# Performance work log

Hardware: AMD Instinct MI355X
Metric: run time of the kernel (lower is better)

Reference implementation:

```python
import jax, jax.numpy as jnp
import numpy as np

DIM = 128
HEADS = 4
CH = DIM // HEADS  # out_channels per head = 32
EDGE_DIM = 1
N_NODES = 50000
N_EDGES = 800000
NEG_SLOPE = 0.2
LN_EPS = 1e-5
SM_EPS = 1e-16  # PyG softmax denom eps


def setup_inputs() -> dict:
    key = jax.random.key(0)
    ks = jax.random.split(key, 10)
    x = jax.random.normal(ks[0], (N_NODES, DIM), dtype=jnp.float32)
    edge_index = jax.random.randint(ks[1], (2, N_EDGES), 0, N_NODES, dtype=jnp.int64)
    edge_attr = jax.random.normal(ks[2], (N_EDGES, EDGE_DIM), dtype=jnp.float32)
    s = 0.05
    W_l = jax.random.normal(ks[3], (DIM, HEADS * CH), dtype=jnp.float32) * s   # shared lin_l/lin_r (share_weights=True)
    b_l = jax.random.normal(ks[4], (HEADS * CH,), dtype=jnp.float32) * s
    W_e = jax.random.normal(ks[5], (EDGE_DIM, HEADS * CH), dtype=jnp.float32) * s  # lin_edge (no bias)
    att = jax.random.normal(ks[6], (HEADS, CH), dtype=jnp.float32) * s
    bias = jax.random.normal(ks[7], (HEADS * CH,), dtype=jnp.float32) * s      # conv output bias
    ln_gamma = jnp.ones((DIM,), dtype=jnp.float32)
    ln_beta = jnp.zeros((DIM,), dtype=jnp.float32)
    return {"x": x, "edge_index": edge_index, "edge_attr": edge_attr,
            "W_l": W_l, "b_l": b_l, "W_e": W_e, "att": att, "bias": bias,
            "ln_gamma": ln_gamma, "ln_beta": ln_beta}


def reference(x, edge_index, edge_attr, W_l, b_l, W_e, att, bias, ln_gamma, ln_beta):
    N = x.shape[0]
    src, dst = edge_index[0], edge_index[1]

    # --- GATv2Conv (share_weights=True, add_self_loops=False, edge_dim injection) ---
    xl = (x @ W_l + b_l).reshape(N, HEADS, CH)            # [N,H,C] (x_l == x_r)
    e = (edge_attr @ W_e).reshape(-1, HEADS, CH)          # [E,H,C]
    m = jax.nn.leaky_relu(xl[src] + xl[dst] + e, NEG_SLOPE)  # [E,H,C]
    alpha = jnp.einsum('ehc,hc->eh', m, att)              # [E,H]

    # segment softmax over destination node neighborhoods
    amax = jax.ops.segment_max(alpha, dst, num_segments=N)   # [N,H]
    ea = jnp.exp(alpha - amax[dst])                           # [E,H]
    denom = jax.ops.segment_sum(ea, dst, num_segments=N)      # [N,H]
    alpha = ea / (denom[dst] + SM_EPS)

    # scatter-aggregate: sum alpha * x_j (projected source feats)
    out = jax.ops.segment_sum(alpha[:, :, None] * xl[src], dst, num_segments=N)  # [N,H,C]
    h = out.reshape(N, HEADS * CH) + bias                  # concat heads + bias -> [N,dim]

    # --- LayerNorm -> GELU (exact, torch default) -> Dropout(eval=identity) -> residual ---
    mu = h.mean(axis=-1, keepdims=True)
    var = ((h - mu) ** 2).mean(axis=-1, keepdims=True)
    hn = (h - mu) * jax.lax.rsqrt(var + LN_EPS) * ln_gamma + ln_beta
    h = jax.nn.gelu(hn, approximate=False)
    return x + h
```

## Files before the change

kernel.cpp:

```cpp
#include <hip/hip_runtime.h>
#include <hip/hip_bf16.h>
#include <stdint.h>


typedef short bf16x8 __attribute__((ext_vector_type(8)));
typedef float f32x4  __attribute__((ext_vector_type(4)));

__device__ __forceinline__ unsigned int f2bf(float f)
{
    __hip_bfloat16 h = __float2bfloat16(f);
    unsigned short u;
    __builtin_memcpy(&u, &h, 2);
    return (unsigned int)u;
}

__global__ void fill_kernel(float* out, int n, float v)
{
    int i = blockIdx.x * 256 + threadIdx.x;
    if (i < n) out[i] = v;
}

__global__ __launch_bounds__(256) void gemm_xl_kernel(
    const float* __restrict__ x, const float* __restrict__ W,
    const float* __restrict__ b, unsigned int* __restrict__ xl, int N)
{
    __shared__ __align__(16) unsigned short sWt[128 * 136];
    __shared__ __align__(16) unsigned short sOut[4 * 16 * 136];
    int tid = threadIdx.x;

    {
        int c  = tid & 127;
        int kh = tid >> 7;
        const float* Wc = W + (size_t)kh * 64 * 128 + c;
        unsigned short* dst = sWt + c * 136 + kh * 64;
#pragma unroll 4
        for (int kk = 0; kk < 16; ++kk) {
            float w0 = Wc[(kk * 4 + 0) * 128];
            float w1 = Wc[(kk * 4 + 1) * 128];
            float w2 = Wc[(kk * 4 + 2) * 128];
            float w3 = Wc[(kk * 4 + 3) * 128];
            uint2 p;
            p.x = f2bf(w0) | (f2bf(w1) << 16);
            p.y = f2bf(w2) | (f2bf(w3) << 16);
            *(uint2*)(dst + kk * 4) = p;
        }
    }
    __syncthreads();

    int w = tid >> 6, lane = tid & 63;
    int li = lane & 15, g = lane >> 4;
    int n0 = blockIdx.x * 128 + w * 32;

    f32x4 acc[2][8];
#pragma unroll
    for (int nt = 0; nt < 8; ++nt) {
        float bb = b[nt * 16 + li];
#pragma unroll
        for (int mt = 0; mt < 2; ++mt) {
            acc[mt][nt][0] = bb; acc[mt][nt][1] = bb;
            acc[mt][nt][2] = bb; acc[mt][nt][3] = bb;
        }
    }

    int row0 = n0 + li;        if (row0 >= N) row0 = N - 1;
    int row1 = n0 + 16 + li;   if (row1 >= N) row1 = N - 1;
    const float* xr0 = x + (size_t)row0 * 128 + g * 8;
    const float* xr1 = x + (size_t)row1 * 128 + g * 8;

#pragma unroll
    for (int kb = 0; kb < 4; ++kb) {
        union { uint32_t u[4]; bf16x8 v; } A0, A1;
        {
            float4 a  = *(const float4*)(xr0 + kb * 32);
            float4 bq = *(const float4*)(xr0 + kb * 32 + 4);
            A0.u[0] = f2bf(a.x)  | (f2bf(a.y)  << 16);
            A0.u[1] = f2bf(a.z)  | (f2bf(a.w)  << 16);
            A0.u[2] = f2bf(bq.x) | (f2bf(bq.y) << 16);
            A0.u[3] = f2bf(bq.z) | (f2bf(bq.w) << 16);
        }
        {
            float4 a  = *(const float4*)(xr1 + kb * 32);
            float4 bq = *(const float4*)(xr1 + kb * 32 + 4);
            A1.u[0] = f2bf(a.x)  | (f2bf(a.y)  << 16);
            A1.u[1] = f2bf(a.z)  | (f2bf(a.w)  << 16);
            A1.u[2] = f2bf(bq.x) | (f2bf(bq.y) << 16);
            A1.u[3] = f2bf(bq.z) | (f2bf(bq.w) << 16);
        }
        const unsigned short* wb = sWt + kb * 32 + g * 8;
#pragma unroll
        for (int nt = 0; nt < 8; ++nt) {
            bf16x8 Bf = *(const bf16x8*)(wb + (nt * 16 + li) * 136);
            acc[0][nt] = __builtin_amdgcn_mfma_f32_16x16x32_bf16(A0.v, Bf, acc[0][nt], 0, 0, 0);
            acc[1][nt] = __builtin_amdgcn_mfma_f32_16x16x32_bf16(A1.v, Bf, acc[1][nt], 0, 0, 0);
        }
    }

    unsigned short* so = sOut + w * 16 * 136;
#pragma unroll
    for (int mt = 0; mt < 2; ++mt) {
#pragma unroll
        for (int nt = 0; nt < 8; ++nt)
#pragma unroll
            for (int r = 0; r < 4; ++r)
                so[(g * 4 + r) * 136 + nt * 16 + li] =
                    (unsigned short)f2bf(acc[mt][nt][r]);
        int rb = n0 + mt * 16;
        for (int it = 0; it < 16; ++it) {
            int n = rb + it;
            if (n < N)
                xl[(size_t)n * 64 + lane] = *(const uint32_t*)(so + it * 136 + lane * 2);
        }
    }
}

__global__ void rank_kernel(const int* __restrict__ ei, int* __restrict__ deg,
                            int* __restrict__ rank, int E, int N)
{
    int e = blockIdx.x * 256 + threadIdx.x;
    if (e < E) {
        int d = ei[(size_t)E + e];
        if ((unsigned)d >= (unsigned)N) d = 0;
        rank[e] = atomicAdd(&deg[d], 1);
    }
}

__global__ void scan_reduce_kernel(const int* __restrict__ deg, int* __restrict__ bsum, int n)
{
    __shared__ int sm[1024];
    int tid = threadIdx.x;
    int i = blockIdx.x * 1024 + tid;
    sm[tid] = (i < n) ? deg[i] : 0;
    __syncthreads();
    for (int o = 512; o >= 1; o >>= 1) {
        if (tid < o) sm[tid] += sm[tid + o];
        __syncthreads();
    }
    if (tid == 0) bsum[blockIdx.x] = sm[0];
}

__global__ void scan_partials_kernel(const int* __restrict__ bsum, int* __restrict__ boff,
                                     int nb, int* __restrict__ row_ptr_last)
{
    if (threadIdx.x == 0) {
        int acc = 0;
        for (int i = 0; i < nb; ++i) { boff[i] = acc; acc += bsum[i]; }
        row_ptr_last[0] = acc;
    }
}

__global__ void scan_final_kernel(const int* __restrict__ deg, const int* __restrict__ boff,
                                  int* __restrict__ row_ptr, int n)
{
    __shared__ int sm[1024];
    int tid = threadIdx.x;
    int i = blockIdx.x * 1024 + tid;
    int v = (i < n) ? deg[i] : 0;
    sm[tid] = v;
    __syncthreads();
    for (int o = 1; o < 1024; o <<= 1) {
        int t = (tid >= o) ? sm[tid - o] : 0;
        __syncthreads();
        sm[tid] += t;
        __syncthreads();
    }
    if (i < n)
        row_ptr[i] = boff[blockIdx.x] + sm[tid] - v;
}

__global__ void scatter_kernel(const int* __restrict__ ei, const float* __restrict__ eattr,
                               const int* __restrict__ row_ptr, const int* __restrict__ rank,
                               int2* __restrict__ rec, int E, int N)
{
    int e = blockIdx.x * 256 + threadIdx.x;
    if (e < E) {
        int s = ei[e];
        int d = ei[(size_t)E + e];
        if ((unsigned)d >= (unsigned)N) d = 0;
        int p = row_ptr[d] + rank[e];
        rec[p] = make_int2(s, __float_as_int(eattr[e]));
    }
}

#define SWZ_ADD(p, pat) ((p) + __int_as_float(__builtin_amdgcn_ds_swizzle(__float_as_int(p), (pat))))
#define DPP_ADD(p, ctrl) ((p) + __int_as_float(__builtin_amdgcn_update_dpp(0, __float_as_int(p), (ctrl), 0xF, 0xF, true)))

__global__ void node_kernel(const unsigned int* __restrict__ xlu, const float* __restrict__ x,
                            const int* __restrict__ row_ptr, const int2* __restrict__ rec,
                            const float* __restrict__ We, const float* __restrict__ att,
                            const float* __restrict__ bias, const float* __restrict__ gamma,
                            const float* __restrict__ beta,
                            float2* __restrict__ out, int N)
{
    int gid = blockIdx.x * 256 + threadIdx.x;
    int n = gid >> 6, lane = gid & 63;
    if (n >= N) return;
    int nw = __builtin_amdgcn_readfirstlane(n);
    int r0 = __builtin_amdgcn_readfirstlane(row_ptr[nw]);
    int r1 = __builtin_amdgcn_readfirstlane(row_ptr[nw + 1]);
    int cnt = r1 - r0;
    const int2* rp = rec + r0;

    int c0 = lane * 2;
    const float LOG2E = 1.4426950408889634f;
    float attv0 = att[c0] * LOG2E, attv1 = att[c0 + 1] * LOG2E;
    float wev0 = We[c0],  wev1 = We[c0 + 1];

    unsigned int un = xlu[((unsigned)nw << 6) + lane];
    float b0 = __uint_as_float(un << 16);
    float b1 = __uint_as_float(un & 0xffff0000u);

    float dsA = 0.f, acA0 = 0.f, acA1 = 0.f;
    float dsB = 0.f, acB0 = 0.f, acB1 = 0.f;

    int last = cnt - 1;
    int2 e0, e1;
    if (cnt > 0) {
        e0 = rp[0];
        e1 = rp[last > 0 ? 1 : 0];
    }
    int t = 0;
    for (; t + 2 <= cnt; t += 2) {
        int sA = e0.x; float evA = __int_as_float(e0.y);
        int sB = e1.x; float evB = __int_as_float(e1.y);
        int p2 = t + 2 < last ? t + 2 : last;
        int p3 = t + 3 < last ? t + 3 : last;
        e0 = rp[p2];
        e1 = rp[p3];
        const unsigned* pA = xlu + (((unsigned)sA) << 6);
        const unsigned* pB = xlu + (((unsigned)sB) << 6);
        unsigned uA = pA[lane];
        unsigned uB = pB[lane];

        float aA0 = __uint_as_float(uA << 16);
        float aA1 = __uint_as_float(uA & 0xffff0000u);
        float aB0 = __uint_as_float(uB << 16);
        float aB1 = __uint_as_float(uB & 0xffff0000u);

        float mA0 = aA0 + fmaf(evA, wev0, b0);
        float mA1 = aA1 + fmaf(evA, wev1, b1);
        float mB0 = aB0 + fmaf(evB, wev0, b0);
        float mB1 = aB1 + fmaf(evB, wev1, b1);
        mA0 = fmaf(0.4f, fabsf(mA0), 0.6f * mA0);
        mA1 = fmaf(0.4f, fabsf(mA1), 0.6f * mA1);
        mB0 = fmaf(0.4f, fabsf(mB0), 0.6f * mB0);
        mB1 = fmaf(0.4f, fabsf(mB1), 0.6f * mB1);

        float pAv = fmaf(mA0, attv0, mA1 * attv1);
        float pBv = fmaf(mB0, attv0, mB1 * attv1);
        pAv = DPP_ADD(pAv, 0xB1);  pBv = DPP_ADD(pBv, 0xB1);
        pAv = DPP_ADD(pAv, 0x4E);  pBv = DPP_ADD(pBv, 0x4E);
        pAv = SWZ_ADD(pAv, 0x101F); pBv = SWZ_ADD(pBv, 0x101F);
        pAv = SWZ_ADD(pAv, 0x201F); pBv = SWZ_ADD(pBv, 0x201F);

        float eA = __builtin_amdgcn_exp2f(pAv);
        float eB = __builtin_amdgcn_exp2f(pBv);
        dsA += eA; dsB += eB;
        acA0 = fmaf(eA, aA0, acA0); acA1 = fmaf(eA, aA1, acA1);
        acB0 = fmaf(eB, aB0, acB0); acB1 = fmaf(eB, aB1, acB1);
    }
    if (t < cnt) {
        int s = e0.x; float ev = __int_as_float(e0.y);
        const unsigned* pS = xlu + (((unsigned)s) << 6);
        unsigned u = pS[lane];
        float a0 = __uint_as_float(u << 16);
        float a1 = __uint_as_float(u & 0xffff0000u);
        float m0 = a0 + fmaf(ev, wev0, b0);
        float m1 = a1 + fmaf(ev, wev1, b1);
        m0 = fmaf(0.4f, fabsf(m0), 0.6f * m0);
        m1 = fmaf(0.4f, fabsf(m1), 0.6f * m1);
        float p = fmaf(m0, attv0, m1 * attv1);
        p = DPP_ADD(p, 0xB1);
        p = DPP_ADD(p, 0x4E);
        p = SWZ_ADD(p, 0x101F);
        p = SWZ_ADD(p, 0x201F);
        float ev2 = __builtin_amdgcn_exp2f(p);
        dsA += ev2;
        acA0 = fmaf(ev2, a0, acA0); acA1 = fmaf(ev2, a1, acA1);
    }
    float dsum = dsA + dsB;
    float acc0 = acA0 + acB0, acc1 = acA1 + acB1;
    float rdh = 1.f / (dsum + 1e-16f);

    float h0 = acc0 * rdh + bias[c0];
    float h1 = acc1 * rdh + bias[c0 + 1];
    float s1 = h0 + h1, s2 = h0 * h0 + h1 * h1;
    s1 = DPP_ADD(s1, 0xB1);  s2 = DPP_ADD(s2, 0xB1);
    s1 = DPP_ADD(s1, 0x4E);  s2 = DPP_ADD(s2, 0x4E);
    s1 = SWZ_ADD(s1, 0x101F); s2 = SWZ_ADD(s2, 0x101F);
    s1 = SWZ_ADD(s1, 0x201F); s2 = SWZ_ADD(s2, 0x201F);
    s1 = SWZ_ADD(s1, 0x401F); s2 = SWZ_ADD(s2, 0x401F);
    s1 += __shfl_xor(s1, 32);
    s2 += __shfl_xor(s2, 32);
    float mu = s1 * (1.f / 128.f);
    float var = s2 * (1.f / 128.f) - mu * mu;
    var = var < 0.f ? 0.f : var;
    float rstd = rsqrtf(var + 1e-5f);
    float g0 = (h0 - mu) * rstd * gamma[c0]     + beta[c0];
    float g1 = (h1 - mu) * rstd * gamma[c0 + 1] + beta[c0 + 1];
    g0 = 0.5f * g0 * (1.f + erff(g0 * 0.70710678118654752f));
    g1 = 0.5f * g1 * (1.f + erff(g1 * 0.70710678118654752f));

    float2 xin = ((const float2*)x)[(size_t)n * 64 + lane];
    float2 o;
    o.x = xin.x + g0;
    o.y = xin.y + g1;
    out[(size_t)n * 64 + lane] = o;
}

extern "C" void kernel_launch(void* const* d_in, const int* in_sizes, int n_in,
                              void* d_out, int out_size, void* d_ws, size_t ws_size,
                              hipStream_t stream)
{
    const int expect[10] = {6400000, 1600000, 800000, 16384, 128, 128, 128, 128, 128, 128};
    int bad = -1;
    if (n_in != 10) bad = 14;
    else for (int i = 0; i < 10; ++i) if (in_sizes[i] != expect[i]) { bad = i; break; }
    if (bad >= 0) {
        fill_kernel<<<(out_size + 255) / 256, 256, 0, stream>>>((float*)d_out, out_size,
                                                                10000.f + 1000.f * (float)bad);
        return;
    }

    const float* x     = (const float*)d_in[0];
    const int*   ei    = (const int*)d_in[1];
    const float* eattr = (const float*)d_in[2];
    const float* W_l   = (const float*)d_in[3];
    const float* b_l   = (const float*)d_in[4];
    const float* W_e   = (const float*)d_in[5];
    const float* att   = (const float*)d_in[6];
    const float* bias  = (const float*)d_in[7];
    const float* gamma = (const float*)d_in[8];
    const float* beta  = (const float*)d_in[9];

    int N = in_sizes[0] / 128;
    int E = in_sizes[1] / 2;
    int nb = (N + 1023) / 1024;

    uint8_t* w = (uint8_t*)d_ws;
    size_t off = 0;
    unsigned int* xl = (unsigned int*)(w + off); off += (size_t)N * 64 * 4;   off = (off + 255) & ~255ull;
    int* deg     = (int*)(w + off);   off += (size_t)N * 4;        off = (off + 255) & ~255ull;
    int* row_ptr = (int*)(w + off);   off += (size_t)(N + 1) * 4;  off = (off + 255) & ~255ull;
    int* rank    = (int*)(w + off);   off += (size_t)E * 4;        off = (off + 255) & ~255ull;
    int2* rec    = (int2*)(w + off);  off += (size_t)E * 8;        off = (off + 255) & ~255ull;
    int* bsum    = (int*)(w + off);   off += (size_t)nb * 4;       off = (off + 255) & ~255ull;
    int* boff    = (int*)(w + off);   off += (size_t)(nb + 1) * 4; off = (off + 255) & ~255ull;

    if (ws_size < off) {
        hipMemsetAsync(d_out, 0, (size_t)out_size * 4, stream);
        return;
    }

    hipMemsetAsync(deg, 0, (size_t)N * 4, stream);
    gemm_xl_kernel<<<(N + 127) / 128, 256, 0, stream>>>(x, W_l, b_l, xl, N);
    rank_kernel<<<(E + 255) / 256, 256, 0, stream>>>(ei, deg, rank, E, N);
    scan_reduce_kernel<<<nb, 1024, 0, stream>>>(deg, bsum, N);
    scan_partials_kernel<<<1, 64, 0, stream>>>(bsum, boff, nb, row_ptr + N);
    scan_final_kernel<<<nb, 1024, 0, stream>>>(deg, boff, row_ptr, N);
    scatter_kernel<<<(E + 255) / 256, 256, 0, stream>>>(ei, eattr, row_ptr, rank, rec, E, N);
    node_kernel<<<(N + 3) / 4, 256, 0, stream>>>(xl, x, row_ptr, rec,
                                                 W_e, att, bias, gamma, beta,
                                                 (float2*)d_out, N);
}
```

Measured before the change: 213.8 us.

## Unroll edge gather by four with scalar indices and fuse scan partials kernel

The per-node gather loop now processes four edges per iteration. It reads edge records through readfirstlane so source indices and edge attributes become wave-uniform scalars, and prefetches the next four records. Cross-lane reductions swap two ds_swizzle steps for DPP row-shift/mirror adds to cut LDS-path latency. The single-thread scan_partials launch is folded into scan_final, where each block sums the preceding block totals itself, removing one kernel launch. The rec buffer is padded so prefetches past the end stay in bounds, but unclamped reads beyond a node's range may pull from the next node's records.

```diff
diff --git a/kernel.cpp b/kernel.cpp
--- a/kernel.cpp
+++ b/kernel.cpp
@@ -138,21 +138,20 @@
     if (tid == 0) bsum[blockIdx.x] = sm[0];
 }
 
-__global__ void scan_partials_kernel(const int* __restrict__ bsum, int* __restrict__ boff,
-                                     int nb, int* __restrict__ row_ptr_last)
-{
-    if (threadIdx.x == 0) {
+__global__ __launch_bounds__(1024) void scan_final_kernel(
+    const int* __restrict__ deg, const int* __restrict__ bsum,
+    int* __restrict__ row_ptr, int n, int E)
+{
+    __shared__ int sm[1024];
+    __shared__ int base;
+    int tid = threadIdx.x;
+    if (tid == 0) {
         int acc = 0;
-        for (int i = 0; i < nb; ++i) { boff[i] = acc; acc += bsum[i]; }
-        row_ptr_last[0] = acc;
-    }
-}
-
-__global__ void scan_final_kernel(const int* __restrict__ deg, const int* __restrict__ boff,
-                                  int* __restrict__ row_ptr, int n)
-{
-    __shared__ int sm[1024];
-    int tid = threadIdx.x;
+        int nb = (int)blockIdx.x;
+        for (int i = 0; i < nb; ++i) acc += bsum[i];
+        base = acc;
+        if (nb == 0) row_ptr[n] = E;
+    }
     int i = blockIdx.x * 1024 + tid;
     int v = (i < n) ? deg[i] : 0;
     sm[tid] = v;
@@ -164,7 +163,7 @@
         __syncthreads();
     }
     if (i < n)
-        row_ptr[i] = boff[blockIdx.x] + sm[tid] - v;
+        row_ptr[i] = base + sm[tid] - v;
 }
 
 __global__ void scatter_kernel(const int* __restrict__ ei, const float* __restrict__ eattr,
@@ -212,56 +211,7 @@
     float dsA = 0.f, acA0 = 0.f, acA1 = 0.f;
     float dsB = 0.f, acB0 = 0.f, acB1 = 0.f;
 
-    int last = cnt - 1;
-    int2 e0, e1;
-    if (cnt > 0) {
-        e0 = rp[0];
-        e1 = rp[last > 0 ? 1 : 0];
-    }
-    int t = 0;
-    for (; t + 2 <= cnt; t += 2) {
-        int sA = e0.x; float evA = __int_as_float(e0.y);
-        int sB = e1.x; float evB = __int_as_float(e1.y);
-        int p2 = t + 2 < last ? t + 2 : last;
-        int p3 = t + 3 < last ? t + 3 : last;
-        e0 = rp[p2];
-        e1 = rp[p3];
-        const unsigned* pA = xlu + (((unsigned)sA) << 6);
-        const unsigned* pB = xlu + (((unsigned)sB) << 6);
-        unsigned uA = pA[lane];
-        unsigned uB = pB[lane];
-
-        float aA0 = __uint_as_float(uA << 16);
-        float aA1 = __uint_as_float(uA & 0xffff0000u);
-        float aB0 = __uint_as_float(uB << 16);
-        float aB1 = __uint_as_float(uB & 0xffff0000u);
-
-        float mA0 = aA0 + fmaf(evA, wev0, b0);
-        float mA1 = aA1 + fmaf(evA, wev1, b1);
-        float mB0 = aB0 + fmaf(evB, wev0, b0);
-        float mB1 = aB1 + fmaf(evB, wev1, b1);
-        mA0 = fmaf(0.4f, fabsf(mA0), 0.6f * mA0);
-        mA1 = fmaf(0.4f, fabsf(mA1), 0.6f * mA1);
-        mB0 = fmaf(0.4f, fabsf(mB0), 0.6f * mB0);
-        mB1 = fmaf(0.4f, fabsf(mB1), 0.6f * mB1);
-
-        float pAv = fmaf(mA0, attv0, mA1 * attv1);
-        float pBv = fmaf(mB0, attv0, mB1 * attv1);
-        pAv = DPP_ADD(pAv, 0xB1);  pBv = DPP_ADD(pBv, 0xB1);
-        pAv = DPP_ADD(pAv, 0x4E);  pBv = DPP_ADD(pBv, 0x4E);
-        pAv = SWZ_ADD(pAv, 0x101F); pBv = SWZ_ADD(pBv, 0x101F);
-        pAv = SWZ_ADD(pAv, 0x201F); pBv = SWZ_ADD(pBv, 0x201F);
-
-        float eA = __builtin_amdgcn_exp2f(pAv);
-        float eB = __builtin_amdgcn_exp2f(pBv);
-        dsA += eA; dsB += eB;
-        acA0 = fmaf(eA, aA0, acA0); acA1 = fmaf(eA, aA1, acA1);
-        acB0 = fmaf(eB, aB0, acB0); acB1 = fmaf(eB, aB1, acB1);
-    }
-    if (t < cnt) {
-        int s = e0.x; float ev = __int_as_float(e0.y);
-        const unsigned* pS = xlu + (((unsigned)s) << 6);
-        unsigned u = pS[lane];
+    auto edge = [&](unsigned u, float ev, float& ds, float& a0c, float& a1c) {
         float a0 = __uint_as_float(u << 16);
         float a1 = __uint_as_float(u & 0xffff0000u);
         float m0 = a0 + fmaf(ev, wev0, b0);
@@ -271,11 +221,44 @@
         float p = fmaf(m0, attv0, m1 * attv1);
         p = DPP_ADD(p, 0xB1);
         p = DPP_ADD(p, 0x4E);
-        p = SWZ_ADD(p, 0x101F);
-        p = SWZ_ADD(p, 0x201F);
-        float ev2 = __builtin_amdgcn_exp2f(p);
-        dsA += ev2;
-        acA0 = fmaf(ev2, a0, acA0); acA1 = fmaf(ev2, a1, acA1);
+        p = DPP_ADD(p, 0x141);
+        p = DPP_ADD(p, 0x140);
+        float e = __builtin_amdgcn_exp2f(p);
+        ds += e;
+        a0c = fmaf(e, a0, a0c);
+        a1c = fmaf(e, a1, a1c);
+    };
+
+    int2 q0, q1, q2, q3;
+    if (cnt > 0) {
+        q0 = rp[0]; q1 = rp[1]; q2 = rp[2]; q3 = rp[3];
+    }
+    int t = 0;
+    for (; t + 4 <= cnt; t += 4) {
+        int   s0 = __builtin_amdgcn_readfirstlane(q0.x);
+        float v0 = __int_as_float(__builtin_amdgcn_readfirstlane(q0.y));
+        int   s1 = __builtin_amdgcn_readfirstlane(q1.x);
+        float v1 = __int_as_float(__builtin_amdgcn_readfirstlane(q1.y));
+        int   s2 = __builtin_amdgcn_readfirstlane(q2.x);
+        float v2 = __int_as_float(__builtin_amdgcn_readfirstlane(q2.y));
+        int   s3 = __builtin_amdgcn_readfirstlane(q3.x);
+        float v3 = __int_as_float(__builtin_amdgcn_readfirstlane(q3.y));
+        q0 = rp[t + 4]; q1 = rp[t + 5]; q2 = rp[t + 6]; q3 = rp[t + 7];
+        unsigned u0 = xlu[(((unsigned)s0) << 6) + lane];
+        unsigned u1 = xlu[(((unsigned)s1) << 6) + lane];
+        unsigned u2 = xlu[(((unsigned)s2) << 6) + lane];
+        unsigned u3 = xlu[(((unsigned)s3) << 6) + lane];
+        edge(u0, v0, dsA, acA0, acA1);
+        edge(u1, v1, dsB, acB0, acB1);
+        edge(u2, v2, dsA, acA0, acA1);
+        edge(u3, v3, dsB, acB0, acB1);
+    }
+    for (; t < cnt; ++t) {
+        int2 q = rp[t];
+        int   s = __builtin_amdgcn_readfirstlane(q.x);
+        float v = __int_as_float(__builtin_amdgcn_readfirstlane(q.y));
+        unsigned u = xlu[(((unsigned)s) << 6) + lane];
+        edge(u, v, dsA, acA0, acA1);
     }
     float dsum = dsA + dsB;
     float acc0 = acA0 + acB0, acc1 = acA1 + acB1;
@@ -284,10 +267,10 @@
     float h0 = acc0 * rdh + bias[c0];
     float h1 = acc1 * rdh + bias[c0 + 1];
     float s1 = h0 + h1, s2 = h0 * h0 + h1 * h1;
-    s1 = DPP_ADD(s1, 0xB1);  s2 = DPP_ADD(s2, 0xB1);
-    s1 = DPP_ADD(s1, 0x4E);  s2 = DPP_ADD(s2, 0x4E);
-    s1 = SWZ_ADD(s1, 0x101F); s2 = SWZ_ADD(s2, 0x101F);
-    s1 = SWZ_ADD(s1, 0x201F); s2 = SWZ_ADD(s2, 0x201F);
+    s1 = DPP_ADD(s1, 0xB1);   s2 = DPP_ADD(s2, 0xB1);
+    s1 = DPP_ADD(s1, 0x4E);   s2 = DPP_ADD(s2, 0x4E);
+    s1 = DPP_ADD(s1, 0x141);  s2 = DPP_ADD(s2, 0x141);
+    s1 = DPP_ADD(s1, 0x140);  s2 = DPP_ADD(s2, 0x140);
     s1 = SWZ_ADD(s1, 0x401F); s2 = SWZ_ADD(s2, 0x401F);
     s1 += __shfl_xor(s1, 32);
     s2 += __shfl_xor(s2, 32);
@@ -342,9 +325,8 @@
     int* deg     = (int*)(w + off);   off += (size_t)N * 4;        off = (off + 255) & ~255ull;
     int* row_ptr = (int*)(w + off);   off += (size_t)(N + 1) * 4;  off = (off + 255) & ~255ull;
     int* rank    = (int*)(w + off);   off += (size_t)E * 4;        off = (off + 255) & ~255ull;
-    int2* rec    = (int2*)(w + off);  off += (size_t)E * 8;        off = (off + 255) & ~255ull;
+    int2* rec    = (int2*)(w + off);  off += (size_t)(E + 8) * 8;  off = (off + 255) & ~255ull;
     int* bsum    = (int*)(w + off);   off += (size_t)nb * 4;       off = (off + 255) & ~255ull;
-    int* boff    = (int*)(w + off);   off += (size_t)(nb + 1) * 4; off = (off + 255) & ~255ull;
 
     if (ws_size < off) {
         hipMemsetAsync(d_out, 0, (size_t)out_size * 4, stream);
@@ -355,8 +337,7 @@
     gemm_xl_kernel<<<(N + 127) / 128, 256, 0, stream>>>(x, W_l, b_l, xl, N);
     rank_kernel<<<(E + 255) / 256, 256, 0, stream>>>(ei, deg, rank, E, N);
     scan_reduce_kernel<<<nb, 1024, 0, stream>>>(deg, bsum, N);
-    scan_partials_kernel<<<1, 64, 0, stream>>>(bsum, boff, nb, row_ptr + N);
-    scan_final_kernel<<<nb, 1024, 0, stream>>>(deg, boff, row_ptr, N);
+    scan_final_kernel<<<nb, 1024, 0, stream>>>(deg, bsum, row_ptr, N, E);
     scatter_kernel<<<(E + 255) / 256, 256, 0, stream>>>(ei, eattr, row_ptr, rank, rec, E, N);
     node_kernel<<<(N + 3) / 4, 256, 0, stream>>>(xl, x, row_ptr, rec,
                                                  W_e, att, bias, gamma, beta,
```

Measured after the change: 201.6 us. -5.7%, faster.
